# Kernel optimization log

Hardware: AMD Instinct MI355X
Metric: run time of the kernel (lower is better)

Reference implementation:

```python
import jax, jax.numpy as jnp
import numpy as np

B, CIN, COUT, H, W, K, KH, KW = 32, 256, 256, 56, 56, 4, 3, 3
STRIDE, PAD = (1, 1), [(1, 1), (1, 1)]


def setup_inputs() -> dict:
    key = jax.random.key(0)
    ks = jax.random.split(key, 8)
    s_w = 1.0 / np.sqrt(CIN * KH * KW)
    return {
        "x": jax.random.normal(ks[0], (B, CIN, H, W), jnp.float32),
        "weight": jax.random.normal(ks[1], (K, COUT, CIN, KH, KW), jnp.float32) * s_w,
        "bias": jax.random.normal(ks[2], (K, COUT), jnp.float32) * s_w,
        "fc1_w": jax.random.normal(ks[3], (K, CIN), jnp.float32) / np.sqrt(CIN),
        "fc1_b": jax.random.normal(ks[4], (K,), jnp.float32) * 0.01,
        "fc2_w": jax.random.normal(ks[5], (K, K), jnp.float32) / np.sqrt(K),
        "fc2_b": jax.random.normal(ks[6], (K,), jnp.float32) * 0.01,
    }


def reference(x, weight, bias, fc1_w, fc1_b, fc2_w, fc2_b):
    # Attention2D: global avg pool -> 1x1 conv (dense) -> relu -> 1x1 conv -> softmax
    pooled = x.mean(axis=(2, 3))                                  # [B, CIN]
    a = jax.nn.relu(jnp.einsum('bc,kc->bk', pooled, fc1_w) + fc1_b)
    att = jax.nn.softmax(jnp.einsum('bk,jk->bj', a, fc2_w) + fc2_b, axis=1)  # [B, K]

    # Aggregate per-sample weights/bias over K experts
    agg_w = jnp.einsum('bk,koihw->boihw', att, weight)            # [B, COUT, CIN, KH, KW]
    agg_b = att @ bias                                            # [B, COUT]

    # Per-sample conv == grouped conv with groups=B in the torch original
    def conv_one(xi, wi):
        return jax.lax.conv_general_dilated(
            xi[None], wi, window_strides=STRIDE, padding=PAD,
            dimension_numbers=('NCHW', 'OIHW', 'NCHW'))[0]

    out = jax.vmap(conv_one)(x, agg_w)                            # [B, COUT, H, W]
    return out + agg_b[:, :, None, None]
```

## Files before the change

### kernel.cpp

```cpp
#include <hip/hip_runtime.h>
#include <hip/hip_bf16.h>
#include <stdint.h>

#define BB   32
#define CIN  256
#define COUT 256
#define HH   56
#define WW   56
#define HW   3136
#define KEXP 4
#define HP   58

typedef __attribute__((ext_vector_type(8))) short  short8;
typedef __attribute__((ext_vector_type(4))) float  floatx4;

__device__ __forceinline__ unsigned short f2bf(float f) {
    uint32_t u = __float_as_uint(f);
    u = (u + 0x7fffu + ((u >> 16) & 1u)) >> 16;
    return (unsigned short)u;
}
__device__ __forceinline__ float bf2f(unsigned short s) {
    return __uint_as_float(((uint32_t)s) << 16);
}
__device__ __forceinline__ uint32_t pack2(float a, float b) {
    return (uint32_t)f2bf(a) | ((uint32_t)f2bf(b) << 16);
}

__device__ __forceinline__ void async_copy16(const void* gsrc, void* ldst) {
    __builtin_amdgcn_global_load_lds(
        (const __attribute__((address_space(1))) unsigned int*)gsrc,
        (__attribute__((address_space(3))) unsigned int*)ldst, 16, 0, 0);
}

__global__ __launch_bounds__(256) void transpose_pool_kernel(
    const float* __restrict__ x,
    unsigned short* __restrict__ xt,
    float* __restrict__ partial)
{
    __shared__ unsigned short tile[CIN * 62];
    const int bx  = blockIdx.x;
    const int b   = bx / HH;
    const int h   = bx % HH;
    const int tid = threadIdx.x;

    const float* xb = x + (size_t)b * CIN * HW + h * WW;

    for (int i = tid; i < CIN * 14; i += 256) {
        const int c  = i / 14;
        const int wv = i % 14;
        const float4 v = *(const float4*)(xb + (size_t)c * HW + wv * 4);
        uint32_t* p = (uint32_t*)&tile[c * 62 + wv * 4];
        p[0] = pack2(v.x, v.y);
        p[1] = pack2(v.z, v.w);
    }
    __syncthreads();

    {
        float s = 0.f;
        #pragma unroll 8
        for (int i = 0; i < WW; ++i) s += bf2f(tile[tid * 62 + i]);
        partial[((size_t)b * HH + h) * CIN + tid] = s;
    }

    unsigned short* row = xt + (((size_t)b * HP + (h + 1)) * HP) * CIN;
    for (int j = tid; j < WW * 128; j += 256) {
        const int w  = j >> 7;
        const int c2 = (j & 127) * 2;
        const uint32_t v = (uint32_t)tile[c2 * 62 + w]
                         | ((uint32_t)tile[(c2 + 1) * 62 + w] << 16);
        *(uint32_t*)&row[(w + 1) * CIN + c2] = v;
    }

    if (tid < 128) {
        ((uint32_t*)&row[0])[tid]          = 0u;
        ((uint32_t*)&row[57 * CIN])[tid]   = 0u;
    }
    if (h == 0) {
        uint32_t* r0  = (uint32_t*)(xt + ((size_t)b * HP + 0)  * HP * CIN);
        uint32_t* r57 = (uint32_t*)(xt + ((size_t)b * HP + 57) * HP * CIN);
        for (int i = tid; i < HP * 128; i += 256) { r0[i] = 0u; r57[i] = 0u; }
    }
}

__global__ __launch_bounds__(256) void attn_kernel(
    const float* __restrict__ partial,
    const float* __restrict__ fc1w,
    const float* __restrict__ fc1b,
    const float* __restrict__ fc2w,
    const float* __restrict__ fc2b,
    float* __restrict__ att)
{
    __shared__ float pl[CIN];
    const int b   = blockIdx.x;
    const int tid = threadIdx.x;

    float s = 0.f;
    const float* pp = partial + (size_t)b * HH * CIN + tid;
    #pragma unroll 8
    for (int h = 0; h < HH; ++h) s += pp[h * CIN];
    pl[tid] = s * (1.0f / (float)HW);
    __syncthreads();

    if (tid < 64) {
        const int lane = tid;
        float sk[KEXP] = {0.f, 0.f, 0.f, 0.f};
        #pragma unroll
        for (int c0 = 0; c0 < CIN; c0 += 64) {
            const float p = pl[c0 + lane];
            #pragma unroll
            for (int k = 0; k < KEXP; ++k) sk[k] += p * fc1w[k * CIN + c0 + lane];
        }
        #pragma unroll
        for (int off = 32; off > 0; off >>= 1) {
            #pragma unroll
            for (int k = 0; k < KEXP; ++k) sk[k] += __shfl_down(sk[k], off);
        }
        if (lane == 0) {
            float a[KEXP];
            #pragma unroll
            for (int k = 0; k < KEXP; ++k) a[k] = fmaxf(sk[k] + fc1b[k], 0.f);
            float z[KEXP], m = -1e30f;
            #pragma unroll
            for (int j = 0; j < KEXP; ++j) {
                float t = fc2b[j];
                #pragma unroll
                for (int k = 0; k < KEXP; ++k) t += a[k] * fc2w[j * KEXP + k];
                z[j] = t;
                m = fmaxf(m, t);
            }
            float den = 0.f;
            #pragma unroll
            for (int j = 0; j < KEXP; ++j) { z[j] = expf(z[j] - m); den += z[j]; }
            const float inv = 1.0f / den;
            #pragma unroll
            for (int j = 0; j < KEXP; ++j) att[b * KEXP + j] = z[j] * inv;
        }
    }
}

__global__ __launch_bounds__(256) void aggw_kernel(
    const float* __restrict__ weight,
    const float* __restrict__ bias,
    const float* __restrict__ att,
    unsigned short* __restrict__ aggw,
    float* __restrict__ aggb)
{
    __shared__ float accw[CIN * 9];
    const int bx  = blockIdx.x;
    const int o   = bx >> 2;
    const int b0  = (bx & 3) * 8;
    const int tid = threadIdx.x;

    float wreg[KEXP][9];
    #pragma unroll
    for (int k = 0; k < KEXP; ++k) {
        const float* wk = weight + (size_t)(k * COUT + o) * (CIN * 9);
        #pragma unroll
        for (int j = 0; j < 9; ++j) wreg[k][j] = wk[j * 256 + tid];
    }
    float bvals[KEXP];
    #pragma unroll
    for (int k = 0; k < KEXP; ++k) bvals[k] = bias[k * COUT + o];

    for (int bi = 0; bi < 8; ++bi) {
        const int b = b0 + bi;
        float av[KEXP];
        #pragma unroll
        for (int k = 0; k < KEXP; ++k) av[k] = att[b * KEXP + k];

        __syncthreads();
        #pragma unroll
        for (int j = 0; j < 9; ++j) {
            float r = 0.f;
            #pragma unroll
            for (int k = 0; k < KEXP; ++k) r += av[k] * wreg[k][j];
            accw[j * 256 + tid] = r;
        }
        __syncthreads();

        for (int i = tid; i < 9 * 128; i += 256) {
            const int j  = i >> 7;
            const int cp = (i & 127) * 2;
            const uint32_t v = pack2(accw[cp * 9 + j], accw[(cp + 1) * 9 + j]);
            *(uint32_t*)&aggw[(((size_t)b * 9 + j) * COUT + o) * CIN + cp] = v;
        }
        if (tid == 0) {
            float sb = 0.f;
            #pragma unroll
            for (int k = 0; k < KEXP; ++k) sb += av[k] * bvals[k];
            aggb[b * COUT + o] = sb;
        }
    }
}

#define MM(AB, AF, BF) do {                                                    \
    __builtin_amdgcn_s_setprio(1);                                             \
    _Pragma("unroll")                                                          \
    for (int mi_ = 0; mi_ < 4; ++mi_)                                          \
        _Pragma("unroll")                                                      \
        for (int ni_ = 0; ni_ < 4; ++ni_)                                      \
            acc[(AB) + mi_][ni_] = __builtin_amdgcn_mfma_f32_16x16x32_bf16(    \
                AF[mi_], BF[ni_], acc[(AB) + mi_][ni_], 0, 0, 0);              \
    __builtin_amdgcn_s_setprio(0);                                             \
} while (0)

#define TILE(BUF, S1A, S1B, S2A, S2B, VMSTMT) do {                             \
    const char* A0_ = lds + (BUF) + lnoff;                                     \
    const char* B0_ = lds + (BUF) + 32768 + lnoff;                             \
    short8 a0[4], a1[4], a2[4], a3[4], b0[4], b1[4];                           \
    _Pragma("unroll")                                                          \
    for (int i_ = 0; i_ < 4; ++i_)                                             \
        a0[i_] = *(const short8*)(A0_ + wm * 8192 + i_ * 1024);                \
    _Pragma("unroll")                                                          \
    for (int i_ = 0; i_ < 4; ++i_)                                             \
        b0[i_] = *(const short8*)(B0_ + wn * 4096 + i_ * 1024);                \
    _Pragma("unroll")                                                          \
    for (int i_ = 0; i_ < 4; ++i_)                                             \
        a1[i_] = *(const short8*)(A0_ + wm * 8192 + 4096 + i_ * 1024);         \
    S1A; S1B;                                                                  \
    MM(0, a0, b0);                                                             \
    _Pragma("unroll")                                                          \
    for (int i_ = 0; i_ < 4; ++i_)                                             \
        a2[i_] = *(const short8*)(A0_ + 16384 + wm * 8192 + 4096 + i_ * 1024); \
    _Pragma("unroll")                                                          \
    for (int i_ = 0; i_ < 4; ++i_)                                             \
        b1[i_] = *(const short8*)(B0_ + 16384 + wn * 4096 + i_ * 1024);        \
    MM(4, a1, b0);                                                             \
    __builtin_amdgcn_sched_barrier(0);                                         \
    __builtin_amdgcn_s_barrier();                                              \
    __builtin_amdgcn_sched_barrier(0);                                         \
    S2A; S2B;                                                                  \
    _Pragma("unroll")                                                          \
    for (int i_ = 0; i_ < 4; ++i_)                                             \
        a3[i_] = *(const short8*)(A0_ + 16384 + wm * 8192 + i_ * 1024);        \
    MM(4, a2, b1);                                                             \
    MM(0, a3, b1);                                                             \
    __builtin_amdgcn_sched_barrier(0);                                         \
    VMSTMT;                                                                    \
    __builtin_amdgcn_s_barrier();                                              \
    __builtin_amdgcn_sched_barrier(0);                                         \
} while (0)

__global__ __launch_bounds__(512, 2) void conv_gemm_kernel(
    const unsigned short* __restrict__ xt,
    const unsigned short* __restrict__ aggw,
    const float* __restrict__ aggb,
    float* __restrict__ out)
{
    __shared__ __attribute__((aligned(128))) char lds[131072];

    const int bx = blockIdx.x;
    const int wg = (bx & 7) * 52 + (bx >> 3);
    const int b  = wg / 13;
    const int p0 = (wg - b * 13) * 256;

    const int tid  = threadIdx.x;
    const int wave = tid >> 6;
    const int lane = tid & 63;
    const int wm   = wave >> 2;
    const int wn   = wave & 3;
    const int m    = lane & 15;
    const int q    = lane >> 4;
    const int lnoff = m * 64 + ((q ^ (m >> 1)) & 3) * 16;

    const char* aggw_b = (const char*)aggw + (size_t)b * (9 * COUT * CIN * 2);
    const char* xt_b   = (const char*)xt   + (size_t)b * (HP * HP * CIN * 2);

    int aoff0, aoff1, boff0, boff1;
    {
        int n = tid, r = n >> 2, u = n & 3, sw = (u ^ (r >> 1)) & 3;
        aoff0 = r * 512 + sw * 16;
        int p = p0 + r; int pv = (p < HW) ? p : 0;
        int h = pv / WW, w = pv - h * WW;
        boff0 = ((h + 1) * HP + (w + 1)) * 512 + sw * 16;

        n = 512 + tid; r = n >> 2; u = n & 3; sw = (u ^ (r >> 1)) & 3;
        aoff1 = r * 512 + sw * 16;
        p = p0 + r; pv = (p < HW) ? p : 0;
        h = pv / WW; w = pv - h * WW;
        boff1 = ((h + 1) * HP + (w + 1)) * 512 + sw * 16;
    }

    auto stageA = [&](int kt, int ks) {
        const int ga = (kt >> 2) * (COUT * CIN * 2) + (kt & 3) * 128 + ks * 64;
        char* d = lds + (kt & 1) * 65536 + ks * 16384 + wave * 1024;
        async_copy16(aggw_b + (size_t)(ga + aoff0), d);
        async_copy16(aggw_b + (size_t)(ga + aoff1), d + 8192);
    };
    auto stageB = [&](int kt, int ks) {
        const int rs = kt >> 2;
        const int gb = ((rs / 3 - 1) * HP + (rs % 3 - 1)) * 512
                     + (kt & 3) * 128 + ks * 64;
        char* d = lds + (kt & 1) * 65536 + 32768 + ks * 16384 + wave * 1024;
        async_copy16(xt_b + (size_t)(gb + boff0), d);
        async_copy16(xt_b + (size_t)(gb + boff1), d + 8192);
    };

    floatx4 acc[8][4];
    #pragma unroll
    for (int a_ = 0; a_ < 8; ++a_)
        #pragma unroll
        for (int n_ = 0; n_ < 4; ++n_)
            #pragma unroll
            for (int e_ = 0; e_ < 4; ++e_) acc[a_][n_][e_] = 0.f;

    stageA(0, 0); stageB(0, 0);
    stageA(0, 1); stageB(0, 1);
    stageA(1, 0); stageB(1, 0);
    __builtin_amdgcn_sched_barrier(0);
    asm volatile("s_waitcnt vmcnt(4)");
    __builtin_amdgcn_sched_barrier(0);
    __builtin_amdgcn_s_barrier();
    __builtin_amdgcn_sched_barrier(0);

    #pragma unroll 1
    for (int i = 0; i < 17; ++i) {
        const int t0 = 2 * i;
        const int t1 = 2 * i + 1;
        TILE(0,
             stageA(t0 + 1, 1), stageB(t0 + 1, 1),
             stageA(t0 + 2, 0), stageB(t0 + 2, 0),
             asm volatile("s_waitcnt vmcnt(4)"));
        TILE(65536,
             stageA(t1 + 1, 1), stageB(t1 + 1, 1),
             stageA(t1 + 2, 0), stageB(t1 + 2, 0),
             asm volatile("s_waitcnt vmcnt(4)"));
    }
    TILE(0,
         stageA(35, 1), stageB(35, 1),
         ((void)0), ((void)0),
         asm volatile("s_waitcnt vmcnt(0)"));
    TILE(65536, ((void)0), ((void)0), ((void)0), ((void)0), ((void)0));

    float* outb = out + (size_t)b * COUT * HW;
    const int g4 = q * 4;
    #pragma unroll
    for (int am = 0; am < 8; ++am) {
        const int o = wm * 128 + am * 16 + g4;
        #pragma unroll
        for (int e = 0; e < 4; ++e) {
            const float bv = aggb[b * COUT + o + e];
            #pragma unroll
            for (int ni = 0; ni < 4; ++ni) {
                const int p = p0 + wn * 64 + ni * 16 + m;
                if (p < HW) outb[(size_t)(o + e) * HW + p] = acc[am][ni][e] + bv;
            }
        }
    }
}

extern "C" void kernel_launch(void* const* d_in, const int* in_sizes, int n_in,
                              void* d_out, int out_size, void* d_ws, size_t ws_size,
                              hipStream_t stream) {
    const float* x      = (const float*)d_in[0];
    const float* weight = (const float*)d_in[1];
    const float* bias   = (const float*)d_in[2];
    const float* fc1w   = (const float*)d_in[3];
    const float* fc1b   = (const float*)d_in[4];
    const float* fc2w   = (const float*)d_in[5];
    const float* fc2b   = (const float*)d_in[6];
    float* out = (float*)d_out;

    char* ws = (char*)d_ws;
    unsigned short* xt      = (unsigned short*)(ws);
    unsigned short* aggw    = (unsigned short*)(ws + 55115776);
    float*          partial = (float*)(ws + 92864512);
    float*          att     = (float*)(ws + 94699520);
    float*          aggb    = (float*)(ws + 94700032);

    transpose_pool_kernel<<<BB * HH, 256, 0, stream>>>(x, xt, partial);
    attn_kernel<<<BB, 256, 0, stream>>>(partial, fc1w, fc1b, fc2w, fc2b, att);
    aggw_kernel<<<COUT * 4, 256, 0, stream>>>(weight, bias, att, aggw, aggb);
    conv_gemm_kernel<<<BB * 13, 512, 0, stream>>>(xt, aggw, aggb, out);
}
```

Before: 353.7 us.

## Replace split-stage software pipeline with simple double-buffered prefetch loop

Replaces the finely interleaved two-tile pipeline, which staged half-tiles mid-compute with partial vmcnt waits and two barriers per tile, with a plain double-buffer loop. Each iteration issues all loads for the next tile, computes the current one, then waits for all loads (vmcnt(0)) and takes a single barrier. This cuts barriers and scheduling complexity but reduces prefetch depth, since each tile's loads must land within one tile's compute, so load latency may show up as stalls.

```diff
diff --git a/kernel.cpp b/kernel.cpp
--- a/kernel.cpp
+++ b/kernel.cpp
@@ -204,41 +204,32 @@
     __builtin_amdgcn_s_setprio(0);                                             \
 } while (0)
 
-#define TILE(BUF, S1A, S1B, S2A, S2B, VMSTMT) do {                             \
-    const char* A0_ = lds + (BUF) + lnoff;                                     \
-    const char* B0_ = lds + (BUF) + 32768 + lnoff;                             \
+#define TILE_COMPUTE(BUFOFF) do {                                              \
+    const char* A0_ = lds + (BUFOFF) + lnoff;                                  \
+    const char* B0_ = lds + (BUFOFF) + 32768 + lnoff;                          \
     short8 a0[4], a1[4], a2[4], a3[4], b0[4], b1[4];                           \
     _Pragma("unroll")                                                          \
     for (int i_ = 0; i_ < 4; ++i_)                                             \
+        b0[i_] = *(const short8*)(B0_ + wn * 4096 + i_ * 1024);                \
+    _Pragma("unroll")                                                          \
+    for (int i_ = 0; i_ < 4; ++i_)                                             \
         a0[i_] = *(const short8*)(A0_ + wm * 8192 + i_ * 1024);                \
-    _Pragma("unroll")                                                          \
-    for (int i_ = 0; i_ < 4; ++i_)                                             \
-        b0[i_] = *(const short8*)(B0_ + wn * 4096 + i_ * 1024);                \
+    MM(0, a0, b0);                                                             \
     _Pragma("unroll")                                                          \
     for (int i_ = 0; i_ < 4; ++i_)                                             \
         a1[i_] = *(const short8*)(A0_ + wm * 8192 + 4096 + i_ * 1024);         \
-    S1A; S1B;                                                                  \
-    MM(0, a0, b0);                                                             \
+    MM(4, a1, b0);                                                             \
+    _Pragma("unroll")                                                          \
+    for (int i_ = 0; i_ < 4; ++i_)                                             \
+        b1[i_] = *(const short8*)(B0_ + 16384 + wn * 4096 + i_ * 1024);        \
     _Pragma("unroll")                                                          \
     for (int i_ = 0; i_ < 4; ++i_)                                             \
         a2[i_] = *(const short8*)(A0_ + 16384 + wm * 8192 + 4096 + i_ * 1024); \
-    _Pragma("unroll")                                                          \
-    for (int i_ = 0; i_ < 4; ++i_)                                             \
-        b1[i_] = *(const short8*)(B0_ + 16384 + wn * 4096 + i_ * 1024);        \
-    MM(4, a1, b0);                                                             \
-    __builtin_amdgcn_sched_barrier(0);                                         \
-    __builtin_amdgcn_s_barrier();                                              \
-    __builtin_amdgcn_sched_barrier(0);                                         \
-    S2A; S2B;                                                                  \
+    MM(4, a2, b1);                                                             \
     _Pragma("unroll")                                                          \
     for (int i_ = 0; i_ < 4; ++i_)                                             \
         a3[i_] = *(const short8*)(A0_ + 16384 + wm * 8192 + i_ * 1024);        \
-    MM(4, a2, b1);                                                             \
     MM(0, a3, b1);                                                             \
-    __builtin_amdgcn_sched_barrier(0);                                         \
-    VMSTMT;                                                                    \
-    __builtin_amdgcn_s_barrier();                                              \
-    __builtin_amdgcn_sched_barrier(0);                                         \
 } while (0)
 
 __global__ __launch_bounds__(512, 2) void conv_gemm_kernel(
@@ -306,31 +297,26 @@
 
     stageA(0, 0); stageB(0, 0);
     stageA(0, 1); stageB(0, 1);
-    stageA(1, 0); stageB(1, 0);
     __builtin_amdgcn_sched_barrier(0);
-    asm volatile("s_waitcnt vmcnt(4)");
-    __builtin_amdgcn_sched_barrier(0);
+    asm volatile("s_waitcnt vmcnt(0)");
     __builtin_amdgcn_s_barrier();
     __builtin_amdgcn_sched_barrier(0);
 
     #pragma unroll 1
-    for (int i = 0; i < 17; ++i) {
-        const int t0 = 2 * i;
-        const int t1 = 2 * i + 1;
-        TILE(0,
-             stageA(t0 + 1, 1), stageB(t0 + 1, 1),
-             stageA(t0 + 2, 0), stageB(t0 + 2, 0),
-             asm volatile("s_waitcnt vmcnt(4)"));
-        TILE(65536,
-             stageA(t1 + 1, 1), stageB(t1 + 1, 1),
-             stageA(t1 + 2, 0), stageB(t1 + 2, 0),
-             asm volatile("s_waitcnt vmcnt(4)"));
-    }
-    TILE(0,
-         stageA(35, 1), stageB(35, 1),
-         ((void)0), ((void)0),
-         asm volatile("s_waitcnt vmcnt(0)"));
-    TILE(65536, ((void)0), ((void)0), ((void)0), ((void)0), ((void)0));
+    for (int t = 0; t < 35; ++t) {
+        const int nt = t + 1;
+        stageA(nt, 0); stageB(nt, 0);
+        stageA(nt, 1); stageB(nt, 1);
+        __builtin_amdgcn_sched_barrier(0);
+
+        TILE_COMPUTE((t & 1) * 65536);
+
+        __builtin_amdgcn_sched_barrier(0);
+        asm volatile("s_waitcnt vmcnt(0)");
+        __builtin_amdgcn_s_barrier();
+        __builtin_amdgcn_sched_barrier(0);
+    }
+    TILE_COMPUTE(65536);
 
     float* outb = out + (size_t)b * COUT * HW;
     const int g4 = q * 4;
```

Result: slower. 369.1 us (+4.3%).
